# Kernel tuning notes

Measured on AMD Instinct MI355X. Metric: run time of the kernel, lower is better.

The kernel has to match this reference:

```python
import jax, jax.numpy as jnp
import numpy as np

B, S, DIM, H = 2, 2048, 1024, 16
DK = DIM // H  # 64
NEG = -10000000000.0


def setup_inputs() -> dict:
    key = jax.random.key(0)
    k1, k2, k3, k4, k5, k6 = jax.random.split(key, 6)
    dec_xs = jax.random.normal(k1, (B, S, DIM), dtype=jnp.float32)
    enc_xs = jax.random.normal(k2, (B, S, DIM), dtype=jnp.float32)
    mask = jax.random.randint(k3, (B, S, S), 0, 2, dtype=jnp.int32)
    # torch Linear weights: out = x @ W.T, bias=False
    sc = 1.0 / np.sqrt(DIM)
    Wq = jax.random.normal(k4, (DIM, DIM), dtype=jnp.float32) * sc
    Wkv = jax.random.normal(k5, (2 * DIM, DIM), dtype=jnp.float32) * sc
    Wo = jax.random.normal(k6, (DIM, DIM), dtype=jnp.float32) * sc
    return {"dec_xs": dec_xs, "enc_xs": enc_xs, "Wq": Wq, "Wkv": Wkv, "Wo": Wo, "mask": mask}


def reference(dec_xs, enc_xs, Wq, Wkv, Wo, mask):
    b, s, dim = enc_xs.shape
    qs = dec_xs @ Wq.T                      # [b,s,dim]  (dropout inactive in eval)
    kv = enc_xs @ Wkv.T                     # [b,s,2*dim]
    ks, vs = jnp.split(kv, 2, axis=-1)
    # head layout: view(b, s, dk, h) -- heads LAST, as in the original
    qs = qs.reshape(b, s, DK, H)
    ks = ks.reshape(b, s, DK, H)
    vs = vs.reshape(b, s, DK, H)
    scores = jnp.einsum('bqdh,bkdh->bqkh', qs, ks) / np.sqrt(DK)
    scores = jnp.where(mask[..., None] == 0, NEG, scores)
    weights = jax.nn.softmax(scores, axis=-2)  # softmax over key axis
    out = jnp.einsum('bqkh,bkdh->bqdh', weights, vs).reshape(b, s, dim)
    return out @ Wo.T
```

## Files before the change

### kernel.cpp

```cpp
#include <hip/hip_runtime.h>
#include <hip/hip_bf16.h>

#define BB 2
#define SS 2048
#define DIMM 1024
#define HH 16
#define DKK 64
#define QSCALE 0.18033688011112042592f

using bf16 = __hip_bfloat16;
typedef __attribute__((ext_vector_type(8))) short v8s;
typedef __attribute__((ext_vector_type(4))) short v4s;
typedef __attribute__((ext_vector_type(4))) float f32x4;
typedef __attribute__((ext_vector_type(16))) float f32x16;

__device__ __forceinline__ void cvt4(const float* __restrict__ s,
                                     bf16* __restrict__ d, int idx) {
  const float4 f = ((const float4*)s)[idx];
  bf16 t[4] = {__float2bfloat16(f.x), __float2bfloat16(f.y),
               __float2bfloat16(f.z), __float2bfloat16(f.w)};
  *(v4s*)(d + (size_t)idx * 4) = *(const v4s*)t;
}

__device__ __forceinline__ int cvt_pk_bf16(float lo, float hi) {
  int r;
  asm("v_cvt_pk_bf16_f32 %0, %1, %2" : "=v"(r) : "v"(lo), "v"(hi));
  return r;
}

__global__ __launch_bounds__(256) void convert_pack_kernel(
    const float* __restrict__ dec, const float* __restrict__ enc,
    const float* __restrict__ Wq, const float* __restrict__ Wkv,
    const float* __restrict__ Wo, const int* __restrict__ mask,
    bf16* __restrict__ decb, bf16* __restrict__ encb, bf16* __restrict__ Wqb,
    bf16* __restrict__ Wkvb, bf16* __restrict__ Wob,
    unsigned long long* __restrict__ mp) {
  const int gid = blockIdx.x * 256 + threadIdx.x;
  const int NT = 256 * 1024;
#pragma unroll
  for (int i = 0; i < 4; ++i) cvt4(dec, decb, gid + i * NT);
#pragma unroll
  for (int i = 0; i < 4; ++i) cvt4(enc, encb, gid + i * NT);
  cvt4(Wq, Wqb, gid);
#pragma unroll
  for (int i = 0; i < 2; ++i) cvt4(Wkv, Wkvb, gid + i * NT);
  {
    const int n = gid >> 8;
    const int c4 = (gid & 255) * 4;
    const int h = c4 >> 6, d0 = c4 & 63;
    const float* src = Wo + (size_t)n * DIMM + h;
    bf16 t[4];
#pragma unroll
    for (int i2 = 0; i2 < 4; ++i2)
      t[i2] = __float2bfloat16(src[(d0 + i2) * 16]);
    *(v4s*)(Wob + (size_t)n * DIMM + c4) = *(const v4s*)t;
  }
  const int lane = threadIdx.x & 63;
  const int wave_id = gid >> 6;
  for (int i = 0; i < 32; ++i) {
    const size_t w = (size_t)wave_id * 32 + i;
    const unsigned long long bm = __ballot(mask[w * 64 + lane] != 0);
    if (lane == 0) {
      const int bb = (int)(w >> 16);
      const int qq = (int)((w >> 5) & 2047);
      const int kc = (int)(w & 31);
      mp[((size_t)bb * 32 + kc) * SS + qq] = bm;
    }
  }
}

__global__ __launch_bounds__(256) void proj_gemm_kernel(
    const bf16* __restrict__ decb, const bf16* __restrict__ encb,
    const bf16* __restrict__ Wqb, const bf16* __restrict__ Wkvb,
    bf16* __restrict__ Qr, bf16* __restrict__ Kr, bf16* __restrict__ Vt) {
  __shared__ __align__(16) bf16 As[128][72];
  __shared__ __align__(16) bf16 Bs[128][72];
  const int t = threadIdx.x;
  const int wave = t >> 6, lane = t & 63;
  const int quad = lane >> 4, l15 = lane & 15;
  const int wm = (wave >> 1) * 64, wn = (wave & 1) * 64;
  const int bx = blockIdx.x;
  const int kind = bx >> 3;
  const int g = bx & 7;
  const int m0 = blockIdx.y * 128;

  const int sr = t >> 2;
  const int sc = (t & 3) * 16;
  const int voff = (kind == 2) ? DIMM : 0;
  const int wr0 = sr * 16 + g * 2 + voff;
  const int wr1 = sr * 16 + g * 2 + 1 + voff;

  const bf16* arow0;
  const bf16* arow1;
  const bf16* brow0;
  const bf16* brow1;
  if (kind == 0) {
    arow0 = decb + (size_t)(m0 + sr) * DIMM;
    arow1 = decb + (size_t)(m0 + sr + 64) * DIMM;
    brow0 = Wqb + (size_t)wr0 * DIMM;
    brow1 = Wqb + (size_t)wr1 * DIMM;
  } else if (kind == 1) {
    arow0 = encb + (size_t)(m0 + sr) * DIMM;
    arow1 = encb + (size_t)(m0 + sr + 64) * DIMM;
    brow0 = Wkvb + (size_t)wr0 * DIMM;
    brow1 = Wkvb + (size_t)wr1 * DIMM;
  } else {
    arow0 = Wkvb + (size_t)wr0 * DIMM;
    arow1 = Wkvb + (size_t)wr1 * DIMM;
    brow0 = encb + (size_t)(m0 + sr) * DIMM;
    brow1 = encb + (size_t)(m0 + sr + 64) * DIMM;
  }

  v8s apf[4], bpf[4];
  auto loadAB = [&](int kc) {
    apf[0] = ((const v8s*)(arow0 + kc + sc))[0];
    apf[1] = ((const v8s*)(arow0 + kc + sc))[1];
    apf[2] = ((const v8s*)(arow1 + kc + sc))[0];
    apf[3] = ((const v8s*)(arow1 + kc + sc))[1];
    bpf[0] = ((const v8s*)(brow0 + kc + sc))[0];
    bpf[1] = ((const v8s*)(brow0 + kc + sc))[1];
    bpf[2] = ((const v8s*)(brow1 + kc + sc))[0];
    bpf[3] = ((const v8s*)(brow1 + kc + sc))[1];
  };

  f32x4 acc[4][4] = {};
  loadAB(0);

  for (int kc = 0; kc < DIMM; kc += 64) {
    __syncthreads();
    *(v8s*)&As[sr][sc] = apf[0];
    *(v8s*)&As[sr][sc + 8] = apf[1];
    *(v8s*)&As[sr + 64][sc] = apf[2];
    *(v8s*)&As[sr + 64][sc + 8] = apf[3];
    *(v8s*)&Bs[sr][sc] = bpf[0];
    *(v8s*)&Bs[sr][sc + 8] = bpf[1];
    *(v8s*)&Bs[sr + 64][sc] = bpf[2];
    *(v8s*)&Bs[sr + 64][sc + 8] = bpf[3];
    if (kc + 64 < DIMM) loadAB(kc + 64);
    __syncthreads();
#pragma unroll
    for (int ks = 0; ks < 2; ++ks) {
      v8s af[4], bfr[4];
#pragma unroll
      for (int i = 0; i < 4; ++i)
        af[i] = *(const v8s*)&As[wm + i * 16 + l15][ks * 32 + quad * 8];
#pragma unroll
      for (int j = 0; j < 4; ++j)
        bfr[j] = *(const v8s*)&Bs[wn + j * 16 + l15][ks * 32 + quad * 8];
#pragma unroll
      for (int i = 0; i < 4; ++i)
#pragma unroll
        for (int j = 0; j < 4; ++j)
          acc[i][j] = __builtin_amdgcn_mfma_f32_16x16x32_bf16(
              af[i], bfr[j], acc[i][j], 0, 0, 0);
    }
  }

#pragma unroll
  for (int i = 0; i < 4; ++i) {
#pragma unroll
    for (int r = 0; r < 4; ++r) {
      const int mm = wm + i * 16 + quad * 4 + r;
#pragma unroll
      for (int j = 0; j < 4; ++j) {
        const int nn = wn + j * 16 + l15;
        const float v = acc[i][j][r];
        if (kind == 0) {
          Qr[(size_t)(m0 + mm) * DIMM + g * 128 + nn] =
              __float2bfloat16(v * QSCALE);
        } else if (kind == 1) {
          Kr[(size_t)(m0 + mm) * DIMM + g * 128 + nn] = __float2bfloat16(v);
        } else {
          const int h = g * 2 + (mm >> 6), d = mm & 63;
          const int sn = m0 + nn;
          const int b = sn >> 11, s = sn & (SS - 1);
          Vt[(((size_t)b * HH + h) * DKK + d) * SS + s] = __float2bfloat16(v);
        }
      }
    }
  }
}

__global__ __launch_bounds__(256) void out_gemm_kernel(
    const bf16* __restrict__ A, const bf16* __restrict__ W,
    float* __restrict__ out) {
  __shared__ __align__(16) bf16 As[128][72];
  __shared__ __align__(16) bf16 Bs[64][72];
  const int t = threadIdx.x;
  const int wave = t >> 6, lane = t & 63;
  const int quad = lane >> 4, l15 = lane & 15;
  const int wm = (wave >> 1) * 64, wn = (wave & 1) * 32;
  const int n0 = blockIdx.x * 64;
  const int m0 = blockIdx.y * 128;
  const int sr = t >> 2;
  const int sc = (t & 3) * 16;

  v8s ar[4], br[2];
  auto loadA = [&](int kc) {
#pragma unroll
    for (int rr = 0; rr < 2; ++rr) {
      const bf16* p = A + (size_t)(m0 + sr + rr * 64) * DIMM + kc + sc;
#pragma unroll
      for (int i = 0; i < 2; ++i) ar[rr * 2 + i] = ((const v8s*)p)[i];
    }
  };
  auto loadB = [&](int kc) {
    const bf16* p = W + (size_t)(n0 + sr) * DIMM + kc + sc;
#pragma unroll
    for (int i = 0; i < 2; ++i) br[i] = ((const v8s*)p)[i];
  };

  f32x4 acc[4][2] = {};
  loadA(0);
  loadB(0);
  for (int kc = 0; kc < DIMM; kc += 64) {
    __syncthreads();
#pragma unroll
    for (int rr = 0; rr < 2; ++rr) {
      *(v8s*)&As[sr + rr * 64][sc] = ar[rr * 2 + 0];
      *(v8s*)&As[sr + rr * 64][sc + 8] = ar[rr * 2 + 1];
    }
    *(v8s*)&Bs[sr][sc] = br[0];
    *(v8s*)&Bs[sr][sc + 8] = br[1];
    if (kc + 64 < DIMM) {
      loadA(kc + 64);
      loadB(kc + 64);
    }
    __syncthreads();
#pragma unroll
    for (int ks = 0; ks < 2; ++ks) {
      v8s af[4], bfr[2];
#pragma unroll
      for (int i = 0; i < 4; ++i)
        af[i] = *(const v8s*)&As[wm + i * 16 + l15][ks * 32 + quad * 8];
#pragma unroll
      for (int j = 0; j < 2; ++j)
        bfr[j] = *(const v8s*)&Bs[wn + j * 16 + l15][ks * 32 + quad * 8];
#pragma unroll
      for (int i = 0; i < 4; ++i)
#pragma unroll
        for (int j = 0; j < 2; ++j)
          acc[i][j] = __builtin_amdgcn_mfma_f32_16x16x32_bf16(
              af[i], bfr[j], acc[i][j], 0, 0, 0);
    }
  }

#pragma unroll
  for (int i = 0; i < 4; ++i) {
#pragma unroll
    for (int r = 0; r < 4; ++r) {
      const int m = m0 + wm + i * 16 + quad * 4 + r;
#pragma unroll
      for (int j = 0; j < 2; ++j) {
        const int n = n0 + wn + j * 16 + l15;
        out[(size_t)m * DIMM + n] = acc[i][j][r];
      }
    }
  }
}

__global__ __launch_bounds__(512) void attn_kernel(
    const bf16* __restrict__ Qr, const bf16* __restrict__ Kr,
    const bf16* __restrict__ Vt, const unsigned long long* __restrict__ mp,
    bf16* __restrict__ Ar) {
  __shared__ __align__(16) bf16 smem[2][2][2][64][72];

  const int t = threadIdx.x;
  const int wave = t >> 6, lane = t & 63;
  const int l31 = lane & 31, hf = lane >> 5;
  const int qb = wave & 3;
  const int pr = wave >> 2;

  const int bx = blockIdx.x;
  const int xcd = bx & 7, j = bx >> 3;
  const int g = (xcd << 2) | (j & 3);
  const int tile = j >> 2;
  const int hd = g & 15, b = g >> 4;

  const int qw = tile * 128 + qb * 32;
  const size_t bhv = ((size_t)b * HH + hd) * DKK;

  v8s bq[4];
  {
    const bf16* qrow = Qr + ((size_t)(b * SS + qw + l31)) * DIMM + hd * 64;
#pragma unroll
    for (int cs = 0; cs < 4; ++cs)
      bq[cs] = *(const v8s*)(qrow + cs * 16 + 8 * hf);
  }

  v8s vones;
#pragma unroll
  for (int i = 0; i < 8; ++i) vones[i] = (short)0x3F80;

  f32x16 o0 = {}, o1 = {}, ol = {};

  const int r0 = t >> 3;
  const int c0 = (t & 7) * 8;

  auto gK = [&](int kt) {
    return *(const v8s*)(Kr + ((size_t)(b * SS + kt * 64 + r0)) * DIMM +
                         hd * 64 + c0);
  };
  auto gV = [&](int kt) {
    return *(const v8s*)(Vt + (bhv + r0) * SS + kt * 64 + c0);
  };
  auto loadM = [&](int kt) {
    return mp[((size_t)b * 32 + kt) * SS + qw + l31];
  };

  {
    const v8s k0 = gK(0), v0 = gV(0), k1 = gK(1), v1 = gV(1);
    *(v8s*)&smem[0][0][0][r0][c0] = k0;
    *(v8s*)&smem[1][0][0][r0][c0] = v0;
    *(v8s*)&smem[0][1][0][r0][c0] = k1;
    *(v8s*)&smem[1][1][0][r0][c0] = v1;
  }
  v8s kpr[2], vpr[2];
  kpr[0] = gK(2);
  vpr[0] = gV(2);
  kpr[1] = gK(3);
  vpr[1] = gV(3);
  unsigned long long mwcur = loadM(pr);

  for (int s = 0; s < 16; ++s) {
    __syncthreads();
    const int nb = (s + 1) & 1;
    if (s < 15) {
      *(v8s*)&smem[0][0][nb][r0][c0] = kpr[0];
      *(v8s*)&smem[1][0][nb][r0][c0] = vpr[0];
      *(v8s*)&smem[0][1][nb][r0][c0] = kpr[1];
      *(v8s*)&smem[1][1][nb][r0][c0] = vpr[1];
      if (s < 14) {
        kpr[0] = gK(2 * s + 4);
        vpr[0] = gV(2 * s + 4);
        kpr[1] = gK(2 * s + 5);
        vpr[1] = gV(2 * s + 5);
      }
    }
    const unsigned long long mwnext = (s < 15) ? loadM(2 * s + 2 + pr) : 0ULL;
    const unsigned long long mq = mwcur >> (4 * hf);
    const int cb = s & 1;

    f32x16 st[2];
#pragma unroll
    for (int n = 0; n < 2; ++n) {
      f32x16 sa = {};
#pragma unroll
      for (int cs = 0; cs < 4; ++cs) {
        const v8s ak =
            *(const v8s*)&smem[0][pr][cb][n * 32 + l31][cs * 16 + 8 * hf];
        sa = __builtin_amdgcn_mfma_f32_32x32x16_bf16(ak, bq[cs], sa, 0, 0, 0);
      }
      st[n] = sa;
    }

    int pd[8][2];
#pragma unroll
    for (int n = 0; n < 2; ++n)
#pragma unroll
      for (int g2 = 0; g2 < 4; ++g2)
#pragma unroll
        for (int jj = 0; jj < 2; ++jj) {
          const int bp = 32 * n + 8 * g2 + 2 * jj;
          const int m = g2 * 4 + 2 * jj;
          const float p0 =
              ((mq >> bp) & 1) ? __builtin_amdgcn_exp2f(st[n][m]) : 0.f;
          const float p1 =
              ((mq >> (bp + 1)) & 1) ? __builtin_amdgcn_exp2f(st[n][m + 1])
                                     : 0.f;
          pd[n * 4 + g2][jj] = cvt_pk_bf16(p0, p1);
        }

    v8s af[4];
#pragma unroll
    for (int ks = 0; ks < 4; ++ks) {
      int a0 = pd[2 * ks][0], b0 = pd[2 * ks + 1][0];
      int a1 = pd[2 * ks][1], b1 = pd[2 * ks + 1][1];
      asm("v_permlane32_swap_b32 %0, %1" : "+v"(a0), "+v"(b0));
      asm("v_permlane32_swap_b32 %0, %1" : "+v"(a1), "+v"(b1));
      int4 w;
      w.x = a0;
      w.y = a1;
      w.z = b0;
      w.w = b1;
      af[ks] = *(v8s*)&w;
    }

#pragma unroll
    for (int ks = 0; ks < 4; ++ks) {
      const v8s bv0 = *(const v8s*)&smem[1][pr][cb][l31][ks * 16 + 8 * hf];
      const v8s bv1 =
          *(const v8s*)&smem[1][pr][cb][32 + l31][ks * 16 + 8 * hf];
      o0 = __builtin_amdgcn_mfma_f32_32x32x16_bf16(af[ks], bv0, o0, 0, 0, 0);
      o1 = __builtin_amdgcn_mfma_f32_32x32x16_bf16(af[ks], bv1, o1, 0, 0, 0);
      ol = __builtin_amdgcn_mfma_f32_32x32x16_bf16(af[ks], vones, ol, 0, 0, 0);
    }
    mwcur = mwnext;
  }

  __syncthreads();
  float* scratch = (float*)&smem[0][0][0][0][0];
  if (wave >= 4) {
    float* dst = scratch + ((size_t)(wave - 4) * 64 + lane) * 52;
#pragma unroll
    for (int i = 0; i < 4; ++i) {
      f32x4 t0 = {o0[4 * i], o0[4 * i + 1], o0[4 * i + 2], o0[4 * i + 3]};
      f32x4 t1 = {o1[4 * i], o1[4 * i + 1], o1[4 * i + 2], o1[4 * i + 3]};
      f32x4 t2 = {ol[4 * i], ol[4 * i + 1], ol[4 * i + 2], ol[4 * i + 3]};
      *(f32x4*)(dst + 4 * i) = t0;
      *(f32x4*)(dst + 16 + 4 * i) = t1;
      *(f32x4*)(dst + 32 + 4 * i) = t2;
    }
  }
  __syncthreads();
  if (wave < 4) {
    const float* src = scratch + ((size_t)wave * 64 + lane) * 52;
#pragma unroll
    for (int m = 0; m < 16; ++m) {
      o0[m] += src[m];
      o1[m] += src[16 + m];
      ol[m] += src[32 + m];
    }
#pragma unroll
    for (int m = 0; m < 16; ++m) {
      const float inv = __builtin_amdgcn_rcpf(ol[m]);
      const int q = qw + (m & 3) + 8 * (m >> 2) + 4 * hf;
      const size_t row = (size_t)b * SS + q;
      Ar[row * DIMM + hd * 64 + l31] = __float2bfloat16(o0[m] * inv);
      Ar[row * DIMM + hd * 64 + 32 + l31] = __float2bfloat16(o1[m] * inv);
    }
  }
}

extern "C" void kernel_launch(void* const* d_in, const int* in_sizes, int n_in,
                              void* d_out, int out_size, void* d_ws,
                              size_t ws_size, hipStream_t stream) {
  const float* dec = (const float*)d_in[0];
  const float* enc = (const float*)d_in[1];
  const float* Wq = (const float*)d_in[2];
  const float* Wkv = (const float*)d_in[3];
  const float* Wo = (const float*)d_in[4];
  const int* mask = (const int*)d_in[5];
  float* out = (float*)d_out;

  bf16* decb = (bf16*)d_out;
  bf16* Wqb = (bf16*)((char*)d_out + ((size_t)2 * SS * DIMM * 2));

  char* ws = (char*)d_ws;
  size_t off = 0;
  bf16* encb = (bf16*)(ws + off);
  bf16* Ar = (bf16*)(ws + off);   off += (size_t)2 * SS * DIMM * 2;
  bf16* Wkvb = (bf16*)(ws + off); off += (size_t)2 * DIMM * DIMM * 2;
  bf16* Wob = (bf16*)(ws + off);  off += (size_t)DIMM * DIMM * 2;
  bf16* Qr = (bf16*)(ws + off);   off += (size_t)2 * SS * DIMM * 2;
  bf16* Kr = (bf16*)(ws + off);   off += (size_t)2 * SS * DIMM * 2;
  bf16* Vt = (bf16*)(ws + off);   off += (size_t)2 * SS * DIMM * 2;
  unsigned long long* mp = (unsigned long long*)(ws + off);

  dim3 blk(256);
  convert_pack_kernel<<<dim3(1024), blk, 0, stream>>>(
      dec, enc, Wq, Wkv, Wo, mask, decb, encb, Wqb, Wkvb, Wob, mp);
  proj_gemm_kernel<<<dim3(24, 32), blk, 0, stream>>>(decb, encb, Wqb, Wkvb, Qr,
                                                     Kr, Vt);
  attn_kernel<<<dim3(512), dim3(512), 0, stream>>>(Qr, Kr, Vt, mp, Ar);
  out_gemm_kernel<<<dim3(16, 32), blk, 0, stream>>>(Ar, Wob, out);
}
```

Baseline: 240.1 us.

## Single-buffer attention K/V tiles and shrink LDS and registers for higher occupancy

```diff
diff --git a/kernel.cpp b/kernel.cpp
--- a/kernel.cpp
+++ b/kernel.cpp
@@ -259,11 +259,11 @@
   }
 }
 
-__global__ __launch_bounds__(512) void attn_kernel(
+__global__ __launch_bounds__(512, 4) void attn_kernel(
     const bf16* __restrict__ Qr, const bf16* __restrict__ Kr,
     const bf16* __restrict__ Vt, const unsigned long long* __restrict__ mp,
     bf16* __restrict__ Ar) {
-  __shared__ __align__(16) bf16 smem[2][2][2][64][72];
+  __shared__ __align__(16) bf16 smem[2][2][64][72];
 
   const int t = threadIdx.x;
   const int wave = t >> 6, lane = t & 63;
@@ -308,55 +308,39 @@
     return mp[((size_t)b * 32 + kt) * SS + qw + l31];
   };
 
-  {
-    const v8s k0 = gK(0), v0 = gV(0), k1 = gK(1), v1 = gV(1);
-    *(v8s*)&smem[0][0][0][r0][c0] = k0;
-    *(v8s*)&smem[1][0][0][r0][c0] = v0;
-    *(v8s*)&smem[0][1][0][r0][c0] = k1;
-    *(v8s*)&smem[1][1][0][r0][c0] = v1;
-  }
-  v8s kpr[2], vpr[2];
-  kpr[0] = gK(2);
-  vpr[0] = gV(2);
-  kpr[1] = gK(3);
-  vpr[1] = gV(3);
+  v8s kreg[2], vreg[2];
+  kreg[0] = gK(0);
+  vreg[0] = gV(0);
+  kreg[1] = gK(1);
+  vreg[1] = gV(1);
   unsigned long long mwcur = loadM(pr);
 
   for (int s = 0; s < 16; ++s) {
     __syncthreads();
-    const int nb = (s + 1) & 1;
+    *(v8s*)&smem[0][0][r0][c0] = kreg[0];
+    *(v8s*)&smem[0][1][r0][c0] = vreg[0];
+    *(v8s*)&smem[1][0][r0][c0] = kreg[1];
+    *(v8s*)&smem[1][1][r0][c0] = vreg[1];
     if (s < 15) {
-      *(v8s*)&smem[0][0][nb][r0][c0] = kpr[0];
-      *(v8s*)&smem[1][0][nb][r0][c0] = vpr[0];
-      *(v8s*)&smem[0][1][nb][r0][c0] = kpr[1];
-      *(v8s*)&smem[1][1][nb][r0][c0] = vpr[1];
-      if (s < 14) {
-        kpr[0] = gK(2 * s + 4);
-        vpr[0] = gV(2 * s + 4);
-        kpr[1] = gK(2 * s + 5);
-        vpr[1] = gV(2 * s + 5);
-      }
+      kreg[0] = gK(2 * s + 2);
+      vreg[0] = gV(2 * s + 2);
+      kreg[1] = gK(2 * s + 3);
+      vreg[1] = gV(2 * s + 3);
     }
     const unsigned long long mwnext = (s < 15) ? loadM(2 * s + 2 + pr) : 0ULL;
+    __syncthreads();
     const unsigned long long mq = mwcur >> (4 * hf);
-    const int cb = s & 1;
-
-    f32x16 st[2];
+
+    int pd[8][2];
 #pragma unroll
     for (int n = 0; n < 2; ++n) {
       f32x16 sa = {};
 #pragma unroll
       for (int cs = 0; cs < 4; ++cs) {
         const v8s ak =
-            *(const v8s*)&smem[0][pr][cb][n * 32 + l31][cs * 16 + 8 * hf];
+            *(const v8s*)&smem[pr][0][n * 32 + l31][cs * 16 + 8 * hf];
         sa = __builtin_amdgcn_mfma_f32_32x32x16_bf16(ak, bq[cs], sa, 0, 0, 0);
       }
-      st[n] = sa;
-    }
-
-    int pd[8][2];
-#pragma unroll
-    for (int n = 0; n < 2; ++n)
 #pragma unroll
       for (int g2 = 0; g2 < 4; ++g2)
 #pragma unroll
@@ -364,12 +348,13 @@
           const int bp = 32 * n + 8 * g2 + 2 * jj;
           const int m = g2 * 4 + 2 * jj;
           const float p0 =
-              ((mq >> bp) & 1) ? __builtin_amdgcn_exp2f(st[n][m]) : 0.f;
+              ((mq >> bp) & 1) ? __builtin_amdgcn_exp2f(sa[m]) : 0.f;
           const float p1 =
-              ((mq >> (bp + 1)) & 1) ? __builtin_amdgcn_exp2f(st[n][m + 1])
+              ((mq >> (bp + 1)) & 1) ? __builtin_amdgcn_exp2f(sa[m + 1])
                                      : 0.f;
           pd[n * 4 + g2][jj] = cvt_pk_bf16(p0, p1);
         }
+    }
 
     v8s af[4];
 #pragma unroll
@@ -388,9 +373,8 @@
 
 #pragma unroll
     for (int ks = 0; ks < 4; ++ks) {
-      const v8s bv0 = *(const v8s*)&smem[1][pr][cb][l31][ks * 16 + 8 * hf];
-      const v8s bv1 =
-          *(const v8s*)&smem[1][pr][cb][32 + l31][ks * 16 + 8 * hf];
+      const v8s bv0 = *(const v8s*)&smem[pr][1][l31][ks * 16 + 8 * hf];
+      const v8s bv1 = *(const v8s*)&smem[pr][1][32 + l31][ks * 16 + 8 * hf];
       o0 = __builtin_amdgcn_mfma_f32_32x32x16_bf16(af[ks], bv0, o0, 0, 0, 0);
       o1 = __builtin_amdgcn_mfma_f32_32x32x16_bf16(af[ks], bv1, o1, 0, 0, 0);
       ol = __builtin_amdgcn_mfma_f32_32x32x16_bf16(af[ks], vones, ol, 0, 0, 0);
@@ -398,29 +382,41 @@
     mwcur = mwnext;
   }
 
+  float* sc4 = (float*)&smem[0][0][0][0];
   __syncthreads();
-  float* scratch = (float*)&smem[0][0][0][0][0];
   if (wave >= 4) {
-    float* dst = scratch + ((size_t)(wave - 4) * 64 + lane) * 52;
+    float* dst = sc4 + ((size_t)(wave - 4) * 64 + lane) * 36;
 #pragma unroll
     for (int i = 0; i < 4; ++i) {
       f32x4 t0 = {o0[4 * i], o0[4 * i + 1], o0[4 * i + 2], o0[4 * i + 3]};
-      f32x4 t1 = {o1[4 * i], o1[4 * i + 1], o1[4 * i + 2], o1[4 * i + 3]};
       f32x4 t2 = {ol[4 * i], ol[4 * i + 1], ol[4 * i + 2], ol[4 * i + 3]};
       *(f32x4*)(dst + 4 * i) = t0;
-      *(f32x4*)(dst + 16 + 4 * i) = t1;
-      *(f32x4*)(dst + 32 + 4 * i) = t2;
+      *(f32x4*)(dst + 16 + 4 * i) = t2;
     }
   }
   __syncthreads();
   if (wave < 4) {
-    const float* src = scratch + ((size_t)wave * 64 + lane) * 52;
+    const float* src = sc4 + ((size_t)wave * 64 + lane) * 36;
 #pragma unroll
     for (int m = 0; m < 16; ++m) {
       o0[m] += src[m];
-      o1[m] += src[16 + m];
-      ol[m] += src[32 + m];
-    }
+      ol[m] += src[16 + m];
+    }
+  }
+  __syncthreads();
+  if (wave >= 4) {
+    float* dst = sc4 + ((size_t)(wave - 4) * 64 + lane) * 36;
+#pragma unroll
+    for (int i = 0; i < 4; ++i) {
+      f32x4 t1 = {o1[4 * i], o1[4 * i + 1], o1[4 * i + 2], o1[4 * i + 3]};
+      *(f32x4*)(dst + 4 * i) = t1;
+    }
+  }
+  __syncthreads();
+  if (wave < 4) {
+    const float* src = sc4 + ((size_t)wave * 64 + lane) * 36;
+#pragma unroll
+    for (int m = 0; m < 16; ++m) o1[m] += src[m];
 #pragma unroll
     for (int m = 0; m < 16; ++m) {
       const float inv = __builtin_amdgcn_rcpf(ol[m]);
```

Result: slower. 245.8 us (+2.4%).
